# Optimization experiments

Hardware: AMD Instinct MI355X
Metric: run time of the kernel (lower is better)

Reference implementation:

```python
import jax, jax.numpy as jnp
import numpy as np

B, T, DM, H, DK, DV = 2, 2048, 1024, 16, 64, 64


def setup_inputs() -> dict:
    key = jax.random.key(0)
    k = jax.random.split(key, 7)
    std_k = np.float32(1.0 / np.sqrt(DK))
    std_v = np.float32(1.0 / np.sqrt(DV))
    return {
        "xq": jax.random.normal(k[0], (B, T, DM), jnp.float32),
        "xk": jax.random.normal(k[1], (B, T, DM), jnp.float32),
        "xv": jax.random.normal(k[2], (B, T, DM), jnp.float32),
        "mask": jnp.ones((B, T), jnp.float32),  # padding mask: 1 = keep
        "w_q": jax.random.normal(k[3], (H, DM, DK), jnp.float32) * std_k,
        "w_k": jax.random.normal(k[4], (H, DM, DK), jnp.float32) * std_k,
        "w_v": jax.random.normal(k[5], (H, DM, DV), jnp.float32) * std_v,
        "w_o": jax.random.normal(k[6], (H * DV, DM), jnp.float32) * np.float32(1.0 / np.sqrt(H * DV)),
        "b_o": jnp.zeros((DM,), jnp.float32),
    }


def reference(xq, xk, xv, mask, w_q, w_k, w_v, w_o, b_o):
    d_k = w_q.shape[-1]
    # per-head projections: [B,T,DM] x [H,DM,DK] -> [B,H,T,DK]
    q = jnp.einsum('bsd,hdk->bhsk', xq, w_q)
    kk = jnp.einsum('btd,hdk->bhtk', xk, w_k)
    v = jnp.einsum('btd,hdv->bhtv', xv, w_v)
    # NOTE: source divides by d_k (not sqrt(d_k)) -- kept faithful
    scores = jnp.einsum('bhsk,bhtk->bhst', q, kk) / jnp.float32(d_k)
    # _padding_mask: multiply by mask broadcast over key dim, then any exact
    # zero (masked OR coincidentally zero score) becomes -inf -- kept faithful
    masked = scores * mask[:, None, None, :]
    scores = jnp.where(masked == 0.0, -jnp.inf, masked)
    attn = jax.nn.softmax(scores, axis=-1)
    out = jnp.einsum('bhst,bhtv->bhsv', attn, v)  # [B,H,T,DV]
    b, h, t, dv = out.shape
    concat = out.transpose(0, 2, 1, 3).reshape(b, t, h * dv)
    return concat @ w_o + b_o
```

## Files before the change

### kernel.cpp

```cpp
#include <hip/hip_runtime.h>
#include <hip/hip_bf16.h>


typedef __attribute__((ext_vector_type(8))) short short8;
typedef __attribute__((ext_vector_type(4))) short short4v;
typedef __attribute__((ext_vector_type(4))) float f32x4;
typedef __attribute__((ext_vector_type(4))) int i32x4;

__device__ __forceinline__ short f2bf(float f) {
  union { float f; unsigned u; } v; v.f = f;
  unsigned r = v.u + 0x7FFFu + ((v.u >> 16) & 1u);
  return (short)(r >> 16);
}

#define GLD_LDS(g, l) __builtin_amdgcn_global_load_lds( \
    (const __attribute__((address_space(1))) void*)(g), \
    (__attribute__((address_space(3))) void*)(l), 16, 0, 0)

__global__ __launch_bounds__(256) void prep_all(
    const float* __restrict__ xq, const float* __restrict__ xk,
    const float* __restrict__ xv, const float* __restrict__ wq,
    const float* __restrict__ wk, const float* __restrict__ wv,
    const float* __restrict__ wo,
    short* __restrict__ Xb, short* __restrict__ Wall, short* __restrict__ Wot)
{
  const int bx = blockIdx.x, tid = threadIdx.x;
  __shared__ float Lt[64][65];
  if (bx < 6144) {
    int z = bx >> 11;
    const float* x = z == 0 ? xq : (z == 1 ? xk : xv);
    size_t i = ((size_t)(bx & 2047) * 256 + tid) * 8;
    f32x4 f0 = *(const f32x4*)(x + i);
    f32x4 f1 = *(const f32x4*)(x + i + 4);
    short8 s;
#pragma unroll
    for (int j = 0; j < 4; j++) { s[j] = f2bf(f0[j]); s[4 + j] = f2bf(f1[j]); }
    *(short8*)(Xb + (size_t)z * 4194304 + i) = s;
  } else if (bx < 6912) {
    int bz = bx - 6144;
    int z = bz >> 8, inner = bz & 255;
    const float* w = z == 0 ? wq : (z == 1 ? wk : wv);
    short* Wt = Wall + (size_t)z * 1048576;
    int h = inner >> 4, d0 = (inner & 15) * 64;
#pragma unroll
    for (int it = 0; it < 4; it++) {
      int e = tid + it * 256;
      int dl = e >> 4, k4 = (e & 15) * 4;
      f32x4 v = *(const f32x4*)(w + ((size_t)(h * 1024 + d0 + dl) * 64) + k4);
#pragma unroll
      for (int j = 0; j < 4; j++) Lt[dl][k4 + j] = v[j];
    }
    __syncthreads();
#pragma unroll
    for (int it = 0; it < 4; it++) {
      int e = tid + it * 256;
      int kl = e >> 4, dq = e & 15;
      short4v s;
#pragma unroll
      for (int j = 0; j < 4; j++) s[j] = f2bf(Lt[dq * 4 + j][kl]);
      *(short4v*)(Wt + (size_t)(h * 64 + kl) * 1024 + d0 + dq * 4) = s;
    }
  } else {
    int bz = bx - 6912;
    int k0 = (bz >> 4) * 64, n0 = (bz & 15) * 64;
#pragma unroll
    for (int it = 0; it < 4; it++) {
      int e = tid + it * 256;
      int kl = e >> 4, n4 = (e & 15) * 4;
      f32x4 v = *(const f32x4*)(wo + (size_t)(k0 + kl) * 1024 + n0 + n4);
#pragma unroll
      for (int j = 0; j < 4; j++) Lt[kl][n4 + j] = v[j];
    }
    __syncthreads();
#pragma unroll
    for (int it = 0; it < 4; it++) {
      int e = tid + it * 256;
      int nl = e >> 4, kq = e & 15;
      short4v s;
#pragma unroll
      for (int j = 0; j < 4; j++) s[j] = f2bf(Lt[kq * 4 + j][nl]);
      *(short4v*)(Wot + (size_t)(n0 + nl) * 1024 + k0 + kq * 4) = s;
    }
  }
}

__global__ __launch_bounds__(256) void proj_qkv2(
    const short* __restrict__ Xb, const short* __restrict__ Wall,
    short* __restrict__ Qb, short* __restrict__ Kt2, short* __restrict__ Vt2)
{
  const int z = blockIdx.z;
  const short* X  = Xb   + (size_t)z * 4194304;
  const short* Wt = Wall + (size_t)z * 1048576;

  const int t0 = blockIdx.x * 128;
  const int n0 = blockIdx.y * 128;
  const int tid = threadIdx.x, w = tid >> 6, lane = tid & 63;
  const int c = lane & 15, q4 = lane >> 4;
  const int wn = (w & 1) * 64, wt = (w >> 1) * 64;
  const int srow = lane >> 2, scol = (lane & 3) * 8;

  __shared__ __align__(16) short Al[128 * 32];
  __shared__ __align__(16) short Bl[128 * 32];

  f32x4 acc[4][4] = {};

  for (int k0 = 0; k0 < 1024; k0 += 32) {
#pragma unroll
    for (int i = 0; i < 2; i++) {
      int rg = (w * 2 + i) * 16;
      GLD_LDS(Wt + (size_t)(n0 + rg + srow) * 1024 + k0 + scol, Al + rg * 32);
      GLD_LDS(X  + (size_t)(t0 + rg + srow) * 1024 + k0 + scol, Bl + rg * 32);
    }
    __syncthreads();
    short8 a[4], bfr[4];
#pragma unroll
    for (int i = 0; i < 4; i++)
      a[i] = *(const short8*)(Al + (wn + i * 16 + c) * 32 + q4 * 8);
#pragma unroll
    for (int j = 0; j < 4; j++)
      bfr[j] = *(const short8*)(Bl + (wt + j * 16 + c) * 32 + q4 * 8);
#pragma unroll
    for (int i = 0; i < 4; i++)
#pragma unroll
      for (int j = 0; j < 4; j++)
        acc[i][j] = __builtin_amdgcn_mfma_f32_16x16x32_bf16(a[i], bfr[j], acc[i][j], 0, 0, 0);
    __syncthreads();
  }

#pragma unroll
  for (int i = 0; i < 4; i++)
#pragma unroll
    for (int j = 0; j < 4; j++) {
      int n = n0 + wn + i * 16 + q4 * 4;
      int trow = t0 + wt + j * 16 + c;
      int b = trow >> 11, t = trow & 2047;
      int h = n >> 6, cc = n & 63;
      int bh = b * 16 + h;
      f32x4 v = acc[i][j];
      short4v pk;
#pragma unroll
      for (int r = 0; r < 4; r++) pk[r] = f2bf(v[r]);
      if (z == 0) {
        *(short4v*)(Qb + (size_t)(bh * 2048 + t) * 64 + cc) = pk;
      } else if (z == 1) {
        int t5 = t & 31, s_ = t5 >> 4, c_ = t5 & 15;
        size_t base = (size_t)bh * 131072 + (t >> 5) * 2048;
        size_t off = base + ((s_ * 2 + (cc >> 5)) * 16 + c_) * 32 +
                     ((cc >> 3) & 3) * 8 + (cc & 7);
        *(short4v*)(Kt2 + off) = pk;
      } else {
        int t5 = t & 31;
        int kp = ((t5 >> 2) & 3) * 8 + ((t5 >> 4) & 1) * 4 + (t5 & 3);
        size_t base = (size_t)bh * 131072 + (t >> 5) * 2048;
#pragma unroll
        for (int r = 0; r < 4; r++)
          Vt2[base + (size_t)(cc + r) * 32 + kp] = pk[r];
      }
    }
}

__global__ __launch_bounds__(256, 2) void attn14(
    const short* __restrict__ Qb, const short* __restrict__ Kt2,
    const short* __restrict__ Vt2, const float* __restrict__ mask,
    short* __restrict__ AO)
{
  const int bh = blockIdx.x;
  const int tblk = blockIdx.y;
  const int b = bh >> 4, h = bh & 15;
  const short* Qh = Qb  + (size_t)bh * 131072;
  const short* Kh = Kt2 + (size_t)bh * 131072;
  const short* Vh = Vt2 + (size_t)bh * 131072;

  const int tid = threadIdx.x, w = tid >> 6, lane = tid & 63;
  const int c = lane & 15, q4 = lane >> 4;
  const int qrow0 = tblk * 128 + w * 32;

  __shared__ __align__(16) short KV2[2][8192];
  __shared__ __align__(16) float cmL[2048];
  __shared__ __align__(16) float cbL[2048];

  const int ch = c * 4 + q4;
  const int rdo = (ch ^ ((ch >> 3) & 3)) * 8;
  const int sch = (lane ^ ((lane >> 3) & 3)) * 8;

  {
    const float LOG2E_64c = 1.44269504088896f * 0.015625f;
    f32x4 m0 = *(const f32x4*)(mask + b * 2048 + tid * 8);
    f32x4 m1 = *(const f32x4*)(mask + b * 2048 + tid * 8 + 4);
    *(f32x4*)(&cmL[tid * 8])     = m0 * LOG2E_64c;
    *(f32x4*)(&cmL[tid * 8 + 4]) = m1 * LOG2E_64c;
    *(f32x4*)(&cbL[tid * 8])     = (m0 - 1.0f) * 240.0f;
    *(f32x4*)(&cbL[tid * 8 + 4]) = (m1 - 1.0f) * 240.0f;
  }

  short8 qa[2][2];
#pragma unroll
  for (int u = 0; u < 2; u++)
#pragma unroll
    for (int dc = 0; dc < 2; dc++)
      qa[u][dc] = *(const short8*)(Qh + (size_t)(qrow0 + u * 16 + c) * 64 + dc * 32 + q4 * 8);

  f32x4 acc[2][4] = {};
  float l[2] = {0.f, 0.f};

  const int g0 = w * 2;

#define STAGE(BI, P) do { \
    const short* s0 = (g0 < 4) ? (Kh + (size_t)(2 * (P)) * 2048 + g0 * 512) \
                               : (Vh + (size_t)(2 * (P)) * 2048 + (g0 - 4) * 512); \
    GLD_LDS(s0 + sch,         &KV2[BI][g0 * 512]); \
    GLD_LDS(s0 + 512 + sch,   &KV2[BI][g0 * 512 + 512]); \
    const short* s1 = (g0 < 4) ? (Kh + (size_t)(2 * (P) + 1) * 2048 + g0 * 512) \
                               : (Vh + (size_t)(2 * (P) + 1) * 2048 + (g0 - 4) * 512); \
    GLD_LDS(s1 + sch,         &KV2[BI][4096 + g0 * 512]); \
    GLD_LDS(s1 + 512 + sch,   &KV2[BI][4096 + g0 * 512 + 512]); \
  } while (0)

#define BODY1(KB, TT) do { \
    const short* Kb = (KB); \
    short8 kf[2][2], va[4]; \
    _Pragma("unroll") \
    for (int s = 0; s < 2; s++) \
      _Pragma("unroll") \
      for (int dc = 0; dc < 2; dc++) \
        kf[s][dc] = *(const short8*)(Kb + (s * 2 + dc) * 512 + rdo); \
    _Pragma("unroll") \
    for (int vs = 0; vs < 4; vs++) \
      va[vs] = *(const short8*)(Kb + 2048 + vs * 512 + rdo); \
    f32x4 st[2][2]; \
    _Pragma("unroll") \
    for (int u = 0; u < 2; u++) \
      _Pragma("unroll") \
      for (int s = 0; s < 2; s++) { \
        f32x4 z = {}; \
        z = __builtin_amdgcn_mfma_f32_16x16x32_bf16(kf[s][0], qa[u][0], z, 0, 0, 0); \
        st[u][s] = __builtin_amdgcn_mfma_f32_16x16x32_bf16(kf[s][1], qa[u][1], z, 0, 0, 0); \
      } \
    f32x4 cm[2], cb[2]; \
    _Pragma("unroll") \
    for (int s = 0; s < 2; s++) { \
      cm[s] = *(const f32x4*)(&cmL[(TT) * 32 + q4 * 4 + s * 16]); \
      cb[s] = *(const f32x4*)(&cbL[(TT) * 32 + q4 * 4 + s * 16]); \
    } \
    _Pragma("unroll") \
    for (int u = 0; u < 2; u++) { \
      unsigned pkd[2][2]; \
      _Pragma("unroll") \
      for (int s = 0; s < 2; s++) { \
        float e0 = __builtin_amdgcn_exp2f(st[u][s][0] * cm[s][0] + cb[s][0]); \
        float e1 = __builtin_amdgcn_exp2f(st[u][s][1] * cm[s][1] + cb[s][1]); \
        float e2 = __builtin_amdgcn_exp2f(st[u][s][2] * cm[s][2] + cb[s][2]); \
        float e3 = __builtin_amdgcn_exp2f(st[u][s][3] * cm[s][3] + cb[s][3]); \
        l[u] += (e0 + e1) + (e2 + e3); \
        unsigned p01, p23; \
        asm("v_cvt_pk_bf16_f32 %0, %1, %2" : "=v"(p01) : "v"(e0), "v"(e1)); \
        asm("v_cvt_pk_bf16_f32 %0, %1, %2" : "=v"(p23) : "v"(e2), "v"(e3)); \
        pkd[s][0] = p01; pkd[s][1] = p23; \
      } \
      union { i32x4 i; short8 s; } pb; \
      pb.i[0] = (int)pkd[0][0]; pb.i[1] = (int)pkd[0][1]; \
      pb.i[2] = (int)pkd[1][0]; pb.i[3] = (int)pkd[1][1]; \
      _Pragma("unroll") \
      for (int vs = 0; vs < 4; vs++) \
        acc[u][vs] = __builtin_amdgcn_mfma_f32_16x16x32_bf16(va[vs], pb.s, acc[u][vs], 0, 0, 0); \
    } \
  } while (0)

#define BODY(BI, P) do { \
    BODY1(&KV2[BI][0],    2 * (P)); \
    BODY1(&KV2[BI][4096], 2 * (P) + 1); \
  } while (0)

  __syncthreads();
  asm volatile("s_waitcnt vmcnt(0)" ::: "memory");
  STAGE(0, 0);
  asm volatile("s_waitcnt vmcnt(0)" ::: "memory");
  __syncthreads();
  int cur = 0;
  for (int p = 0; p < 31; ++p) {
    STAGE(cur ^ 1, p + 1);
    BODY(cur, p);
    asm volatile("s_waitcnt vmcnt(0)" ::: "memory");
    __syncthreads();
    cur ^= 1;
  }
  BODY(cur, 31);
#undef STAGE
#undef BODY1
#undef BODY

#pragma unroll
  for (int u = 0; u < 2; u++) {
    float lu = l[u];
    lu += __shfl_xor(lu, 16);
    lu += __shfl_xor(lu, 32);
    float inv = 1.0f / lu;
    size_t row = (size_t)b * 2048 + qrow0 + u * 16 + c;
#pragma unroll
    for (int vs = 0; vs < 4; vs++) {
      f32x4 v = acc[u][vs];
      short4v pk;
#pragma unroll
      for (int r = 0; r < 4; r++) pk[r] = f2bf(v[r] * inv);
      *(short4v*)(AO + row * 1024 + h * 64 + vs * 16 + q4 * 4) = pk;
    }
  }
}

__global__ __launch_bounds__(256) void out_proj2(
    const short* __restrict__ AO, const short* __restrict__ Wot,
    const float* __restrict__ bo, float* __restrict__ out)
{
  const int t0 = blockIdx.x * 128;
  const int n0 = blockIdx.y * 128;
  const int tid = threadIdx.x, w = tid >> 6, lane = tid & 63;
  const int c = lane & 15, q4 = lane >> 4;
  const int wn = (w & 1) * 64, wt = (w >> 1) * 64;
  const int srow = lane >> 2, scol = (lane & 3) * 8;

  __shared__ __align__(16) short Al[128 * 32];
  __shared__ __align__(16) short Bl[128 * 32];

  f32x4 acc[4][4] = {};

  for (int k0 = 0; k0 < 1024; k0 += 32) {
#pragma unroll
    for (int i = 0; i < 2; i++) {
      int rg = (w * 2 + i) * 16;
      GLD_LDS(Wot + (size_t)(n0 + rg + srow) * 1024 + k0 + scol, Al + rg * 32);
      GLD_LDS(AO  + (size_t)(t0 + rg + srow) * 1024 + k0 + scol, Bl + rg * 32);
    }
    __syncthreads();
    short8 a[4], bfr[4];
#pragma unroll
    for (int i = 0; i < 4; i++)
      a[i] = *(const short8*)(Al + (wn + i * 16 + c) * 32 + q4 * 8);
#pragma unroll
    for (int j = 0; j < 4; j++)
      bfr[j] = *(const short8*)(Bl + (wt + j * 16 + c) * 32 + q4 * 8);
#pragma unroll
    for (int i = 0; i < 4; i++)
#pragma unroll
      for (int j = 0; j < 4; j++)
        acc[i][j] = __builtin_amdgcn_mfma_f32_16x16x32_bf16(a[i], bfr[j], acc[i][j], 0, 0, 0);
    __syncthreads();
  }

#pragma unroll
  for (int i = 0; i < 4; i++)
#pragma unroll
    for (int j = 0; j < 4; j++) {
      int n = n0 + wn + i * 16 + q4 * 4;
      int trow = t0 + wt + j * 16 + c;
      f32x4 v = acc[i][j] + *(const f32x4*)(bo + n);
      *(f32x4*)(out + (size_t)trow * 1024 + n) = v;
    }
}

extern "C" void kernel_launch(void* const* d_in, const int* in_sizes, int n_in,
                              void* d_out, int out_size, void* d_ws, size_t ws_size,
                              hipStream_t stream)
{
  (void)in_sizes; (void)n_in; (void)out_size; (void)ws_size;
  const float* xq   = (const float*)d_in[0];
  const float* xk   = (const float*)d_in[1];
  const float* xv   = (const float*)d_in[2];
  const float* mask = (const float*)d_in[3];
  const float* wq   = (const float*)d_in[4];
  const float* wk   = (const float*)d_in[5];
  const float* wv   = (const float*)d_in[6];
  const float* wo   = (const float*)d_in[7];
  const float* bo   = (const float*)d_in[8];
  float* out = (float*)d_out;

  char* ws = (char*)d_ws;
  short* Wall = (short*)(ws + (size_t)0);
  short* Wot  = (short*)(ws + ((size_t)6 << 20));
  short* Xb   = (short*)(ws + ((size_t)8 << 20));
  short* AO   = (short*)(ws + ((size_t)8 << 20));
  short* Qb   = (short*)(ws + ((size_t)32 << 20));
  short* Kt2  = (short*)(ws + ((size_t)40 << 20));
  short* Vt2  = (short*)(ws + ((size_t)48 << 20));

  prep_all<<<7168, 256, 0, stream>>>(xq, xk, xv, wq, wk, wv, wo, Xb, Wall, Wot);
  proj_qkv2<<<dim3(32, 8, 3), 256, 0, stream>>>(Xb, Wall, Qb, Kt2, Vt2);
  attn14<<<dim3(32, 16), 256, 0, stream>>>(Qb, Kt2, Vt2, mask, AO);
  out_proj2<<<dim3(32, 8), 256, 0, stream>>>(AO, Wot, bo, out);
}
```

Baseline: 220.4 us.

## Double-buffer GEMM LDS tiles with 64-wide K steps and vectorize V stores

Both projection GEMMs now double-buffer their LDS tiles and take K steps of 64 instead of 32. The global-to-LDS loads for the next stage are issued before the MFMA work on the current stage, and the loop needs half as many barriers. For the V projection the A and B operands are swapped, so each lane holds four consecutive t values and writes them with one packed 4-short store instead of four scalar scattered stores. LDS use per block grows fourfold, to 64KB, which may lower occupancy.

After: 217.9 us. About the same (-1.1%).

```diff
diff --git a/kernel.cpp b/kernel.cpp
--- a/kernel.cpp
+++ b/kernel.cpp
@@ -84,7 +84,7 @@
   }
 }
 
-__global__ __launch_bounds__(256) void proj_qkv2(
+__global__ __launch_bounds__(256) void proj_qkv3(
     const short* __restrict__ Xb, const short* __restrict__ Wall,
     short* __restrict__ Qb, short* __restrict__ Kt2, short* __restrict__ Vt2)
 {
@@ -99,64 +99,109 @@
   const int wn = (w & 1) * 64, wt = (w >> 1) * 64;
   const int srow = lane >> 2, scol = (lane & 3) * 8;
 
-  __shared__ __align__(16) short Al[128 * 32];
-  __shared__ __align__(16) short Bl[128 * 32];
+  __shared__ __align__(16) short Al[2][2][4096];
+  __shared__ __align__(16) short Bl[2][2][4096];
 
   f32x4 acc[4][4] = {};
 
-  for (int k0 = 0; k0 < 1024; k0 += 32) {
-#pragma unroll
-    for (int i = 0; i < 2; i++) {
-      int rg = (w * 2 + i) * 16;
-      GLD_LDS(Wt + (size_t)(n0 + rg + srow) * 1024 + k0 + scol, Al + rg * 32);
-      GLD_LDS(X  + (size_t)(t0 + rg + srow) * 1024 + k0 + scol, Bl + rg * 32);
-    }
+#define PSTAGE(BUF, K0) do { \
+    _Pragma("unroll") \
+    for (int sub = 0; sub < 2; sub++) { \
+      _Pragma("unroll") \
+      for (int i = 0; i < 2; i++) { \
+        int rg = (w * 2 + i) * 16; \
+        GLD_LDS(Wt + (size_t)(n0 + rg + srow) * 1024 + (K0) + sub * 32 + scol, &Al[BUF][sub][rg * 32]); \
+        GLD_LDS(X  + (size_t)(t0 + rg + srow) * 1024 + (K0) + sub * 32 + scol, &Bl[BUF][sub][rg * 32]); \
+      } \
+    } \
+  } while (0)
+
+#define PCOMP(BUF) do { \
+    _Pragma("unroll") \
+    for (int sub = 0; sub < 2; sub++) { \
+      short8 a[4], bfr[4]; \
+      if (z != 2) { \
+        _Pragma("unroll") \
+        for (int i = 0; i < 4; i++) \
+          a[i] = *(const short8*)(&Al[BUF][sub][(wn + i * 16 + c) * 32 + q4 * 8]); \
+        _Pragma("unroll") \
+        for (int j = 0; j < 4; j++) \
+          bfr[j] = *(const short8*)(&Bl[BUF][sub][(wt + j * 16 + c) * 32 + q4 * 8]); \
+      } else { \
+        _Pragma("unroll") \
+        for (int i = 0; i < 4; i++) \
+          a[i] = *(const short8*)(&Bl[BUF][sub][(wt + i * 16 + c) * 32 + q4 * 8]); \
+        _Pragma("unroll") \
+        for (int j = 0; j < 4; j++) \
+          bfr[j] = *(const short8*)(&Al[BUF][sub][(wn + j * 16 + c) * 32 + q4 * 8]); \
+      } \
+      _Pragma("unroll") \
+      for (int i = 0; i < 4; i++) \
+        _Pragma("unroll") \
+        for (int j = 0; j < 4; j++) \
+          acc[i][j] = __builtin_amdgcn_mfma_f32_16x16x32_bf16(a[i], bfr[j], acc[i][j], 0, 0, 0); \
+    } \
+  } while (0)
+
+  PSTAGE(0, 0);
+  asm volatile("s_waitcnt vmcnt(0)" ::: "memory");
+  __syncthreads();
+  int cur = 0;
+  for (int p = 0; p < 15; ++p) {
+    PSTAGE(cur ^ 1, (p + 1) * 64);
+    PCOMP(cur);
+    asm volatile("s_waitcnt vmcnt(0)" ::: "memory");
     __syncthreads();
-    short8 a[4], bfr[4];
+    cur ^= 1;
+  }
+  PCOMP(cur);
+#undef PSTAGE
+#undef PCOMP
+
+  if (z != 2) {
 #pragma unroll
     for (int i = 0; i < 4; i++)
-      a[i] = *(const short8*)(Al + (wn + i * 16 + c) * 32 + q4 * 8);
-#pragma unroll
-    for (int j = 0; j < 4; j++)
-      bfr[j] = *(const short8*)(Bl + (wt + j * 16 + c) * 32 + q4 * 8);
+#pragma unroll
+      for (int j = 0; j < 4; j++) {
+        int n = n0 + wn + i * 16 + q4 * 4;
+        int trow = t0 + wt + j * 16 + c;
+        int b = trow >> 11, t = trow & 2047;
+        int h = n >> 6, cc = n & 63;
+        int bh = b * 16 + h;
+        f32x4 v = acc[i][j];
+        short4v pk;
+#pragma unroll
+        for (int r = 0; r < 4; r++) pk[r] = f2bf(v[r]);
+        if (z == 0) {
+          *(short4v*)(Qb + (size_t)(bh * 2048 + t) * 64 + cc) = pk;
+        } else {
+          int t5 = t & 31, s_ = t5 >> 4, c_ = t5 & 15;
+          size_t base = (size_t)bh * 131072 + (t >> 5) * 2048;
+          size_t off = base + ((s_ * 2 + (cc >> 5)) * 16 + c_) * 32 +
+                       ((cc >> 3) & 3) * 8 + (cc & 7);
+          *(short4v*)(Kt2 + off) = pk;
+        }
+      }
+  } else {
 #pragma unroll
     for (int i = 0; i < 4; i++)
 #pragma unroll
-      for (int j = 0; j < 4; j++)
-        acc[i][j] = __builtin_amdgcn_mfma_f32_16x16x32_bf16(a[i], bfr[j], acc[i][j], 0, 0, 0);
-    __syncthreads();
-  }
-
-#pragma unroll
-  for (int i = 0; i < 4; i++)
-#pragma unroll
-    for (int j = 0; j < 4; j++) {
-      int n = n0 + wn + i * 16 + q4 * 4;
-      int trow = t0 + wt + j * 16 + c;
-      int b = trow >> 11, t = trow & 2047;
-      int h = n >> 6, cc = n & 63;
-      int bh = b * 16 + h;
-      f32x4 v = acc[i][j];
-      short4v pk;
-#pragma unroll
-      for (int r = 0; r < 4; r++) pk[r] = f2bf(v[r]);
-      if (z == 0) {
-        *(short4v*)(Qb + (size_t)(bh * 2048 + t) * 64 + cc) = pk;
-      } else if (z == 1) {
-        int t5 = t & 31, s_ = t5 >> 4, c_ = t5 & 15;
+      for (int j = 0; j < 4; j++) {
+        int tq = t0 + wt + i * 16 + q4 * 4;
+        int n = n0 + wn + j * 16 + c;
+        int b = tq >> 11, t = tq & 2047;
+        int h = n >> 6, cc = n & 63;
+        int bh = b * 16 + h;
+        int t5 = t & 31;
+        int kpb = ((t5 >> 2) & 3) * 8 + ((t5 >> 4) & 1) * 4;
         size_t base = (size_t)bh * 131072 + (t >> 5) * 2048;
-        size_t off = base + ((s_ * 2 + (cc >> 5)) * 16 + c_) * 32 +
-                     ((cc >> 3) & 3) * 8 + (cc & 7);
-        *(short4v*)(Kt2 + off) = pk;
-      } else {
-        int t5 = t & 31;
-        int kp = ((t5 >> 2) & 3) * 8 + ((t5 >> 4) & 1) * 4 + (t5 & 3);
-        size_t base = (size_t)bh * 131072 + (t >> 5) * 2048;
-#pragma unroll
-        for (int r = 0; r < 4; r++)
-          Vt2[base + (size_t)(cc + r) * 32 + kp] = pk[r];
+        f32x4 v = acc[i][j];
+        short4v pk;
+#pragma unroll
+        for (int r = 0; r < 4; r++) pk[r] = f2bf(v[r]);
+        *(short4v*)(Vt2 + base + (size_t)cc * 32 + kpb) = pk;
       }
-    }
+  }
 }
 
 __global__ __launch_bounds__(256, 2) void attn14(
@@ -307,7 +352,7 @@
   }
 }
 
-__global__ __launch_bounds__(256) void out_proj2(
+__global__ __launch_bounds__(256) void out_proj3(
     const short* __restrict__ AO, const short* __restrict__ Wot,
     const float* __restrict__ bo, float* __restrict__ out)
 {
@@ -318,33 +363,55 @@
   const int wn = (w & 1) * 64, wt = (w >> 1) * 64;
   const int srow = lane >> 2, scol = (lane & 3) * 8;
 
-  __shared__ __align__(16) short Al[128 * 32];
-  __shared__ __align__(16) short Bl[128 * 32];
+  __shared__ __align__(16) short Al[2][2][4096];
+  __shared__ __align__(16) short Bl[2][2][4096];
 
   f32x4 acc[4][4] = {};
 
-  for (int k0 = 0; k0 < 1024; k0 += 32) {
-#pragma unroll
-    for (int i = 0; i < 2; i++) {
-      int rg = (w * 2 + i) * 16;
-      GLD_LDS(Wot + (size_t)(n0 + rg + srow) * 1024 + k0 + scol, Al + rg * 32);
-      GLD_LDS(AO  + (size_t)(t0 + rg + srow) * 1024 + k0 + scol, Bl + rg * 32);
-    }
+#define PSTAGE(BUF, K0) do { \
+    _Pragma("unroll") \
+    for (int sub = 0; sub < 2; sub++) { \
+      _Pragma("unroll") \
+      for (int i = 0; i < 2; i++) { \
+        int rg = (w * 2 + i) * 16; \
+        GLD_LDS(Wot + (size_t)(n0 + rg + srow) * 1024 + (K0) + sub * 32 + scol, &Al[BUF][sub][rg * 32]); \
+        GLD_LDS(AO  + (size_t)(t0 + rg + srow) * 1024 + (K0) + sub * 32 + scol, &Bl[BUF][sub][rg * 32]); \
+      } \
+    } \
+  } while (0)
+
+#define PCOMP(BUF) do { \
+    _Pragma("unroll") \
+    for (int sub = 0; sub < 2; sub++) { \
+      short8 a[4], bfr[4]; \
+      _Pragma("unroll") \
+      for (int i = 0; i < 4; i++) \
+        a[i] = *(const short8*)(&Al[BUF][sub][(wn + i * 16 + c) * 32 + q4 * 8]); \
+      _Pragma("unroll") \
+      for (int j = 0; j < 4; j++) \
+        bfr[j] = *(const short8*)(&Bl[BUF][sub][(wt + j * 16 + c) * 32 + q4 * 8]); \
+      _Pragma("unroll") \
+      for (int i = 0; i < 4; i++) \
+        _Pragma("unroll") \
+        for (int j = 0; j < 4; j++) \
+          acc[i][j] = __builtin_amdgcn_mfma_f32_16x16x32_bf16(a[i], bfr[j], acc[i][j], 0, 0, 0); \
+    } \
+  } while (0)
+
+  PSTAGE(0, 0);
+  asm volatile("s_waitcnt vmcnt(0)" ::: "memory");
+  __syncthreads();
+  int cur = 0;
+  for (int p = 0; p < 15; ++p) {
+    PSTAGE(cur ^ 1, (p + 1) * 64);
+    PCOMP(cur);
+    asm volatile("s_waitcnt vmcnt(0)" ::: "memory");
     __syncthreads();
-    short8 a[4], bfr[4];
-#pragma unroll
-    for (int i = 0; i < 4; i++)
-      a[i] = *(const short8*)(Al + (wn + i * 16 + c) * 32 + q4 * 8);
-#pragma unroll
-    for (int j = 0; j < 4; j++)
-      bfr[j] = *(const short8*)(Bl + (wt + j * 16 + c) * 32 + q4 * 8);
-#pragma unroll
-    for (int i = 0; i < 4; i++)
-#pragma unroll
-      for (int j = 0; j < 4; j++)
-        acc[i][j] = __builtin_amdgcn_mfma_f32_16x16x32_bf16(a[i], bfr[j], acc[i][j], 0, 0, 0);
-    __syncthreads();
-  }
+    cur ^= 1;
+  }
+  PCOMP(cur);
+#undef PSTAGE
+#undef PCOMP
 
 #pragma unroll
   for (int i = 0; i < 4; i++)
@@ -383,7 +450,7 @@
   short* Vt2  = (short*)(ws + ((size_t)48 << 20));
 
   prep_all<<<7168, 256, 0, stream>>>(xq, xk, xv, wq, wk, wv, wo, Xb, Wall, Wot);
-  proj_qkv2<<<dim3(32, 8, 3), 256, 0, stream>>>(Xb, Wall, Qb, Kt2, Vt2);
+  proj_qkv3<<<dim3(32, 8, 3), 256, 0, stream>>>(Xb, Wall, Qb, Kt2, Vt2);
   attn14<<<dim3(32, 16), 256, 0, stream>>>(Qb, Kt2, Vt2, mask, AO);
-  out_proj2<<<dim3(32, 8), 256, 0, stream>>>(AO, Wot, bo, out);
-}
+  out_proj3<<<dim3(32, 8), 256, 0, stream>>>(AO, Wot, bo, out);
+}
```
